# Kernel tuning notes

Hardware: AMD Instinct MI355X
Metric: run time of the kernel (lower is better)

The kernel has to match this reference:

```python
import jax, jax.numpy as jnp
import numpy as np

B, S, D_IN, D_H = 8, 2048, 768, 1024

def _linear_params(key, d_in, d_out):
    kw, kb = jax.random.split(key)
    bound = 1.0 / np.sqrt(d_in)
    W = jax.random.uniform(kw, (d_in, d_out), jnp.float32, -bound, bound)
    b = jax.random.uniform(kb, (d_out,), jnp.float32, -bound, bound)
    return W, b

def setup_inputs() -> dict:
    key = jax.random.key(0)
    ks = jax.random.split(key, 6)
    x = jax.random.normal(ks[0], (B, S, D_IN), jnp.float32)
    W1, b1 = _linear_params(ks[1], D_IN, D_H)
    Wq, bq = _linear_params(ks[2], D_H, D_H)
    Wk, bk = _linear_params(ks[3], D_H, D_H)
    Wv, bv = _linear_params(ks[4], D_H, D_H)
    W2, b2 = _linear_params(ks[5], D_H, D_H)
    Ws, bs = _linear_params(jax.random.fold_in(key, 7), D_IN, D_H)
    return {"x": x, "W1": W1, "b1": b1, "Wq": Wq, "bq": bq, "Wk": Wk, "bk": bk,
            "Wv": Wv, "bv": bv, "W2": W2, "b2": b2, "Ws": Ws, "bs": bs}

def reference(x, W1, b1, Wq, bq, Wk, bk, Wv, bv, W2, b2, Ws, bs):
    h = jax.nn.relu(x @ W1 + b1)                      # [B,S,D_H]
    q = h @ Wq + bq
    k = h @ Wk + bk
    v = h @ Wv + bv
    scale = 1.0 / jnp.sqrt(jnp.float32(h.shape[-1]))
    attn = jax.nn.softmax(jnp.einsum('bsd,btd->bst', q, k) * scale, axis=-1)
    h = jnp.einsum('bst,btd->bsd', attn, v)
    h = h + (x @ Ws + bs)                             # shortcut (input_dim != hidden_dim)
    return jax.nn.relu(h @ W2 + b2)
```

## Files before the change

### kernel.cpp

```cpp
#include <hip/hip_runtime.h>
#include <cstdint>
#include <cstddef>

#define BB   8
#define SS   2048
#define DIN  768
#define DHID 1024

typedef unsigned short u16;
typedef __bf16 bf16x8 __attribute__((ext_vector_type(8)));
typedef float  f32x4  __attribute__((ext_vector_type(4)));

__device__ __forceinline__ u16 f2bf(float f) {
  unsigned u = __float_as_uint(f);
  return (u16)((u + 0x7fffu + ((u >> 16) & 1u)) >> 16);
}
__device__ __forceinline__ float bf2f(u16 h) {
  return __uint_as_float((unsigned)h << 16);
}

#define GLOAD16(g, l)                                                         \
  __builtin_amdgcn_global_load_lds(                                           \
      (const __attribute__((address_space(1))) unsigned int*)(g),             \
      (__attribute__((address_space(3))) unsigned int*)(l), 16, 0, 0)

template <int OUT_MODE, bool RELU, bool HASRES>
__global__ __launch_bounds__(512, 2)
void gemm256(const u16* __restrict__ A, const u16* __restrict__ B,
             const float* __restrict__ bias, const u16* __restrict__ res,
             void* __restrict__ Cv, int M, int N, int K, float alpha,
             long strA, long strB, long strC) {
  __shared__ u16 sA[4][8192];
  __shared__ u16 sB[4][8192];

  const int nbx = gridDim.x, nby = gridDim.y;
  const long nwg  = (long)nbx * nby * gridDim.z;
  const long orig = blockIdx.x + (long)nbx * (blockIdx.y + (long)nby * blockIdx.z);
  const long per  = nwg >> 3;
  const long swz  = (orig & 7) * per + (orig >> 3);
  const int  bz   = (int)(swz / ((long)nbx * nby));
  const int  rem  = (int)(swz % ((long)nbx * nby));
  const int  by   = rem / nbx, bx = rem % nbx;

  A += (long)bz * strA;
  B += (long)bz * strB;

  const int tid  = threadIdx.x;
  const int lane = tid & 63;
  const int w    = tid >> 6;
  const int wr   = w >> 2;
  const int wc   = w & 3;
  const int bm0  = by * 256;
  const int bn0  = bx * 256;

  const int sr    = lane >> 2;
  const int clog  = ((lane & 3) * 8) ^ (((lane >> 2) & 6) << 2);
  const u16* AgBase = A + (long)(bm0 + w * 32 + sr) * K + clog;
  const u16* BgBase = B + (long)(bn0 + w * 32 + sr) * K + clog;

  const int fr = lane & 15;
  const int fk = (lane >> 4) * 8;
  const int ck = fk ^ ((fr & 6) << 2);

  f32x4 acc[8][4] = {};
  const int T = K >> 5;

  auto stage = [&](int t) {
    const int bf_ = t & 3;
    const long k0 = (long)t * 32;
    u16* la = &sA[bf_][(w * 32) * 32];
    u16* lb = &sB[bf_][(w * 32) * 32];
    GLOAD16(AgBase + k0,                 la);
    GLOAD16(AgBase + k0 + 16 * (long)K,  la + 16 * 32);
    GLOAD16(BgBase + k0,                 lb);
    GLOAD16(BgBase + k0 + 16 * (long)K,  lb + 16 * 32);
  };

  stage(0); stage(1); stage(2);
  asm volatile("s_waitcnt vmcnt(8)" ::: "memory");
  __builtin_amdgcn_s_barrier();
  __builtin_amdgcn_sched_barrier(0);

  for (int t = 0; t < T; ++t) {
    if (t + 3 < T) stage(t + 3);

    const int b = t & 3;
    bf16x8 af[8], bfv[4];
#pragma unroll
    for (int m = 0; m < 8; ++m)
      af[m] = *(const bf16x8*)(&sA[b][(wr * 128 + m * 16 + fr) * 32 + ck]);
#pragma unroll
    for (int n = 0; n < 4; ++n)
      bfv[n] = *(const bf16x8*)(&sB[b][(wc * 64 + n * 16 + fr) * 32 + ck]);

    asm volatile("s_waitcnt lgkmcnt(0)" ::: "memory");
    if (t + 3 < T)      asm volatile("s_waitcnt vmcnt(8)" ::: "memory");
    else if (t + 2 < T) asm volatile("s_waitcnt vmcnt(4)" ::: "memory");
    else                asm volatile("s_waitcnt vmcnt(0)" ::: "memory");
    __builtin_amdgcn_s_barrier();
    __builtin_amdgcn_sched_barrier(0);

    __builtin_amdgcn_s_setprio(1);
#pragma unroll
    for (int m = 0; m < 8; ++m)
#pragma unroll
      for (int n = 0; n < 4; ++n)
        acc[m][n] = __builtin_amdgcn_mfma_f32_16x16x32_bf16(af[m], bfv[n],
                                                            acc[m][n], 0, 0, 0);
    __builtin_amdgcn_s_setprio(0);
  }

#pragma unroll
  for (int m = 0; m < 8; ++m) {
    const int row0 = bm0 + wr * 128 + m * 16 + (lane >> 4) * 4;
#pragma unroll
    for (int n = 0; n < 4; ++n) {
      const int col = bn0 + wc * 64 + n * 16 + fr;
      f32x4 v = acc[m][n];
      const float bvv = bias ? bias[col] : 0.f;
#pragma unroll
      for (int r = 0; r < 4; ++r) {
        float val = v[r] * alpha + bvv;
        if (HASRES) val += bf2f(res[(long)(row0 + r) * N + col]);
        if (RELU)   val = fmaxf(val, 0.f);
        v[r] = val;
      }
      if (OUT_MODE == 0) {
        u16* C = (u16*)Cv + (long)bz * strC;
#pragma unroll
        for (int r = 0; r < 4; ++r)
          C[(long)(row0 + r) * N + col] = f2bf(v[r]);
      } else if (OUT_MODE == 1) {
        const int bb = row0 >> 11;
        const int s0 = row0 & 2047;
        u16* C = (u16*)Cv + (long)bb * (SS * DHID) + (long)col * SS + s0;
        ushort4 p;
        p.x = f2bf(v[0]); p.y = f2bf(v[1]); p.z = f2bf(v[2]); p.w = f2bf(v[3]);
        *(ushort4*)C = p;
      } else {
        float* C = (float*)Cv + (long)bz * strC;
#pragma unroll
        for (int r = 0; r < 4; ++r)
          C[(long)(row0 + r) * N + col] = v[r];
      }
    }
  }
}

__device__ __forceinline__ float waveReduce(float v, bool isMax) {
#pragma unroll
  for (int off = 32; off > 0; off >>= 1) {
    float o = __shfl_xor(v, off);
    v = isMax ? fmaxf(v, o) : (v + o);
  }
  return v;
}

__global__ __launch_bounds__(256)
void softmax2048b(u16* __restrict__ sc) {
  __shared__ float red[4];
  u16* row = sc + (size_t)blockIdx.x * 2048;
  const int tid = threadIdx.x;
  const int wv = tid >> 6, lane = tid & 63;

  uint4 raw = ((const uint4*)row)[tid];
  u16* us = (u16*)&raw;
  float f[8];
#pragma unroll
  for (int i = 0; i < 8; ++i) f[i] = bf2f(us[i]);

  float mx = f[0];
#pragma unroll
  for (int i = 1; i < 8; ++i) mx = fmaxf(mx, f[i]);
  mx = waveReduce(mx, true);
  if (lane == 0) red[wv] = mx;
  __syncthreads();
  mx = fmaxf(fmaxf(red[0], red[1]), fmaxf(red[2], red[3]));
  __syncthreads();

  float s = 0.f;
#pragma unroll
  for (int i = 0; i < 8; ++i) { f[i] = __expf(f[i] - mx); s += f[i]; }
  s = waveReduce(s, false);
  if (lane == 0) red[wv] = s;
  __syncthreads();
  s = red[0] + red[1] + red[2] + red[3];
  const float inv = 1.f / s;

#pragma unroll
  for (int i = 0; i < 8; ++i) us[i] = f2bf(f[i] * inv);
  ((uint4*)row)[tid] = raw;
}

__global__ __launch_bounds__(256)
void cvt8(const float* __restrict__ in, u16* __restrict__ out, long n) {
  long i = ((long)blockIdx.x * 256 + threadIdx.x) * 8;
  if (i >= n) return;
  float4 a = *(const float4*)(in + i);
  float4 b = *(const float4*)(in + i + 4);
  uint4 o;
  u16* us = (u16*)&o;
  us[0] = f2bf(a.x); us[1] = f2bf(a.y); us[2] = f2bf(a.z); us[3] = f2bf(a.w);
  us[4] = f2bf(b.x); us[5] = f2bf(b.y); us[6] = f2bf(b.z); us[7] = f2bf(b.w);
  *(uint4*)(out + i) = o;
}

__global__ __launch_bounds__(256)
void wtrans(const float* __restrict__ W, u16* __restrict__ WT, int K, int N) {
  __shared__ float t[32][33];
  const int tx = threadIdx.x & 31, ty = threadIdx.x >> 5;
  const int n0 = blockIdx.x * 32, k0 = blockIdx.y * 32;
#pragma unroll
  for (int r = 0; r < 32; r += 8)
    t[ty + r][tx] = W[(long)(k0 + ty + r) * N + n0 + tx];
  __syncthreads();
#pragma unroll
  for (int r = 0; r < 32; r += 8)
    WT[(long)(n0 + ty + r) * K + k0 + tx] = f2bf(t[tx][ty + r]);
}

extern "C" void kernel_launch(void* const* d_in, const int* in_sizes, int n_in,
                              void* d_out, int out_size, void* d_ws, size_t ws_size,
                              hipStream_t stream) {
  const float* x  = (const float*)d_in[0];
  const float* W1 = (const float*)d_in[1];
  const float* b1 = (const float*)d_in[2];
  const float* Wq = (const float*)d_in[3];
  const float* bq = (const float*)d_in[4];
  const float* Wk = (const float*)d_in[5];
  const float* bk = (const float*)d_in[6];
  const float* Wv = (const float*)d_in[7];
  const float* bv = (const float*)d_in[8];
  const float* W2 = (const float*)d_in[9];
  const float* b2 = (const float*)d_in[10];
  const float* Wsm = (const float*)d_in[11];
  const float* bs = (const float*)d_in[12];
  float* out = (float*)d_out;

  const long M   = (long)BB * SS;
  const long MD  = M * DHID;
  const long SD  = (long)SS * DHID;
  const long SSq = (long)SS * SS;
  const long NX  = M * DIN;

  u16* wsb = (u16*)d_ws;
  u16* xb  = wsb;
  u16* W1T = xb  + NX;
  u16* WqT = W1T + (long)DHID * DIN;
  u16* WkT = WqT + (long)DHID * DHID;
  u16* WvT = WkT + (long)DHID * DHID;
  u16* W2T = WvT + (long)DHID * DHID;
  u16* WsT = W2T + (long)DHID * DHID;
  u16* h   = WsT + (long)DHID * DIN;
  u16* q   = h + MD;
  u16* k   = q + MD;
  u16* scores = k + MD;
  u16* vT  = (u16*)d_out;

  long avail = (long)(ws_size / 2) - (scores - wsb);
  int nb = (int)(avail / SSq);
  if (nb > BB) nb = BB;
  if (nb < 1) nb = 1;

  cvt8<<<(unsigned)((NX / 8 + 255) / 256), 256, 0, stream>>>(x, xb, NX);
  wtrans<<<dim3(DHID / 32, DIN / 32), 256, 0, stream>>>(W1, W1T, DIN, DHID);
  wtrans<<<dim3(DHID / 32, DHID / 32), 256, 0, stream>>>(Wq, WqT, DHID, DHID);
  wtrans<<<dim3(DHID / 32, DHID / 32), 256, 0, stream>>>(Wk, WkT, DHID, DHID);
  wtrans<<<dim3(DHID / 32, DHID / 32), 256, 0, stream>>>(Wv, WvT, DHID, DHID);
  wtrans<<<dim3(DHID / 32, DHID / 32), 256, 0, stream>>>(W2, W2T, DHID, DHID);
  wtrans<<<dim3(DHID / 32, DIN / 32), 256, 0, stream>>>(Wsm, WsT, DIN, DHID);

  const dim3 gMain(DHID / 256, M / 256, 1);

  gemm256<0, true, false><<<gMain, 512, 0, stream>>>(
      xb, W1T, b1, nullptr, h, (int)M, DHID, DIN, 1.f, 0, 0, 0);
  gemm256<0, false, false><<<gMain, 512, 0, stream>>>(
      h, WqT, bq, nullptr, q, (int)M, DHID, DHID, 1.f, 0, 0, 0);
  gemm256<0, false, false><<<gMain, 512, 0, stream>>>(
      h, WkT, bk, nullptr, k, (int)M, DHID, DHID, 1.f, 0, 0, 0);
  gemm256<1, false, false><<<gMain, 512, 0, stream>>>(
      h, WvT, bv, nullptr, vT, (int)M, DHID, DHID, 1.f, 0, 0, 0);

  const float scale = 0.03125f;
  for (int b0 = 0; b0 < BB; b0 += nb) {
    const int cb = (b0 + nb <= BB) ? nb : (BB - b0);
    gemm256<0, false, false><<<dim3(SS / 256, SS / 256, cb), 512, 0, stream>>>(
        q + (long)b0 * SD, k + (long)b0 * SD, nullptr, nullptr, scores,
        SS, SS, DHID, scale, SD, SD, SSq);
    softmax2048b<<<cb * SS, 256, 0, stream>>>(scores);
    gemm256<0, false, false><<<dim3(DHID / 256, SS / 256, cb), 512, 0, stream>>>(
        scores, vT + (long)b0 * SD, nullptr, nullptr, h + (long)b0 * SD,
        SS, DHID, SS, 1.f, SSq, SD, SD);
  }

  gemm256<0, false, true><<<gMain, 512, 0, stream>>>(
      xb, WsT, bs, h, q, (int)M, DHID, DIN, 1.f, 0, 0, 0);

  gemm256<2, true, false><<<gMain, 512, 0, stream>>>(
      q, W2T, b2, nullptr, out, (int)M, DHID, DHID, 1.f, 0, 0, 0);
}
```

Measured before the change: 602.2 us.

## Restructure GEMM main loop into double-buffered 64-K stages with interleaved quarter-tile MFMA phases

Replaces the 4-deep 32-K circular LDS buffer with a 2-slot buffer of 64-K steps, each split into two 32-K halves. Each half is computed in two MFMA phases, and the next tile's A and B loads are issued between phases, so global-to-LDS traffic is spread across the iteration. Fragment registers are halved (af[4] instead of af[8]) and the launch-bounds occupancy hint of 2 is dropped. This should cut register pressure and overlap loads with compute more finely. The cost is many more barriers per iteration and a shallower prefetch distance, which may expose memory latency.

```diff
diff --git a/kernel.cpp b/kernel.cpp
--- a/kernel.cpp
+++ b/kernel.cpp
@@ -24,14 +24,17 @@
       (const __attribute__((address_space(1))) unsigned int*)(g),             \
       (__attribute__((address_space(3))) unsigned int*)(l), 16, 0, 0)
 
+#define SB0()  __builtin_amdgcn_sched_barrier(0)
+#define BAR()  __builtin_amdgcn_s_barrier()
+
 template <int OUT_MODE, bool RELU, bool HASRES>
-__global__ __launch_bounds__(512, 2)
+__global__ __launch_bounds__(512)
 void gemm256(const u16* __restrict__ A, const u16* __restrict__ B,
              const float* __restrict__ bias, const u16* __restrict__ res,
              void* __restrict__ Cv, int M, int N, int K, float alpha,
              long strA, long strB, long strC) {
-  __shared__ u16 sA[4][8192];
-  __shared__ u16 sB[4][8192];
+  __shared__ u16 sA[2][2][8192];
+  __shared__ u16 sB[2][2][8192];
 
   const int nbx = gridDim.x, nby = gridDim.y;
   const long nwg  = (long)nbx * nby * gridDim.z;
@@ -53,61 +56,111 @@
   const int bm0  = by * 256;
   const int bn0  = bx * 256;
 
-  const int sr    = lane >> 2;
-  const int clog  = ((lane & 3) * 8) ^ (((lane >> 2) & 6) << 2);
-  const u16* AgBase = A + (long)(bm0 + w * 32 + sr) * K + clog;
-  const u16* BgBase = B + (long)(bn0 + w * 32 + sr) * K + clog;
+  const int sr   = lane >> 2;
+  const int clog = ((lane & 3) * 8) ^ (((lane >> 2) & 6) << 2);
+  const u16* Ag = A + (long)(bm0 + w * 32 + sr) * K + clog;
+  const u16* Bg = B + (long)(bn0 + w * 32 + sr) * K + clog;
 
   const int fr = lane & 15;
   const int fk = (lane >> 4) * 8;
   const int ck = fk ^ ((fr & 6) << 2);
+  const int aoff = (wr * 128 + fr) * 32 + ck;
+  const int boff = (wc * 64  + fr) * 32 + ck;
+
+  auto stageA = [&](int slot, int ks, int t) {
+    u16* d = &sA[slot][ks][(w * 32) * 32];
+    const u16* g = Ag + (long)t * 64 + ks * 32;
+    GLOAD16(g, d);
+    GLOAD16(g + 16 * (long)K, d + 512);
+  };
+  auto stageB = [&](int slot, int ks, int t) {
+    u16* d = &sB[slot][ks][(w * 32) * 32];
+    const u16* g = Bg + (long)t * 64 + ks * 32;
+    GLOAD16(g, d);
+    GLOAD16(g + 16 * (long)K, d + 512);
+  };
 
   f32x4 acc[8][4] = {};
-  const int T = K >> 5;
-
-  auto stage = [&](int t) {
-    const int bf_ = t & 3;
-    const long k0 = (long)t * 32;
-    u16* la = &sA[bf_][(w * 32) * 32];
-    u16* lb = &sB[bf_][(w * 32) * 32];
-    GLOAD16(AgBase + k0,                 la);
-    GLOAD16(AgBase + k0 + 16 * (long)K,  la + 16 * 32);
-    GLOAD16(BgBase + k0,                 lb);
-    GLOAD16(BgBase + k0 + 16 * (long)K,  lb + 16 * 32);
-  };
-
-  stage(0); stage(1); stage(2);
-  asm volatile("s_waitcnt vmcnt(8)" ::: "memory");
-  __builtin_amdgcn_s_barrier();
-  __builtin_amdgcn_sched_barrier(0);
+  bf16x8 af[4], bfv[4];
+  const int T = K >> 6;
+
+  stageA(0, 0, 0); stageB(0, 0, 0); stageA(0, 1, 0); stageB(0, 1, 0);
+  asm volatile("s_waitcnt vmcnt(4)" ::: "memory");
+  BAR(); SB0();
 
   for (int t = 0; t < T; ++t) {
-    if (t + 3 < T) stage(t + 3);
-
-    const int b = t & 3;
-    bf16x8 af[8], bfv[4];
-#pragma unroll
-    for (int m = 0; m < 8; ++m)
-      af[m] = *(const bf16x8*)(&sA[b][(wr * 128 + m * 16 + fr) * 32 + ck]);
+    const int s = t & 1, s1 = s ^ 1;
+    const bool pf = (t + 1 < T);
+
+#pragma unroll
+    for (int m = 0; m < 4; ++m)
+      af[m] = *(const bf16x8*)(&sA[s][0][aoff + m * 512]);
 #pragma unroll
     for (int n = 0; n < 4; ++n)
-      bfv[n] = *(const bf16x8*)(&sB[b][(wc * 64 + n * 16 + fr) * 32 + ck]);
-
-    asm volatile("s_waitcnt lgkmcnt(0)" ::: "memory");
-    if (t + 3 < T)      asm volatile("s_waitcnt vmcnt(8)" ::: "memory");
-    else if (t + 2 < T) asm volatile("s_waitcnt vmcnt(4)" ::: "memory");
-    else                asm volatile("s_waitcnt vmcnt(0)" ::: "memory");
-    __builtin_amdgcn_s_barrier();
-    __builtin_amdgcn_sched_barrier(0);
-
+      bfv[n] = *(const bf16x8*)(&sB[s][0][boff + n * 512]);
+    if (pf) stageA(s1, 0, t + 1);
+    SB0(); BAR(); SB0();
     __builtin_amdgcn_s_setprio(1);
 #pragma unroll
-    for (int m = 0; m < 8; ++m)
+    for (int m = 0; m < 4; ++m)
 #pragma unroll
       for (int n = 0; n < 4; ++n)
         acc[m][n] = __builtin_amdgcn_mfma_f32_16x16x32_bf16(af[m], bfv[n],
                                                             acc[m][n], 0, 0, 0);
     __builtin_amdgcn_s_setprio(0);
+    BAR(); SB0();
+
+#pragma unroll
+    for (int m = 0; m < 4; ++m)
+      af[m] = *(const bf16x8*)(&sA[s][0][aoff + (m + 4) * 512]);
+    if (pf) stageB(s1, 0, t + 1);
+    SB0(); BAR(); SB0();
+    __builtin_amdgcn_s_setprio(1);
+#pragma unroll
+    for (int m = 0; m < 4; ++m)
+#pragma unroll
+      for (int n = 0; n < 4; ++n)
+        acc[m + 4][n] = __builtin_amdgcn_mfma_f32_16x16x32_bf16(af[m], bfv[n],
+                                                                acc[m + 4][n], 0, 0, 0);
+    __builtin_amdgcn_s_setprio(0);
+    if (pf) asm volatile("s_waitcnt vmcnt(4)" ::: "memory");
+    else    asm volatile("s_waitcnt vmcnt(0)" ::: "memory");
+    BAR(); SB0();
+
+#pragma unroll
+    for (int m = 0; m < 4; ++m)
+      af[m] = *(const bf16x8*)(&sA[s][1][aoff + m * 512]);
+#pragma unroll
+    for (int n = 0; n < 4; ++n)
+      bfv[n] = *(const bf16x8*)(&sB[s][1][boff + n * 512]);
+    if (pf) stageA(s1, 1, t + 1);
+    SB0(); BAR(); SB0();
+    __builtin_amdgcn_s_setprio(1);
+#pragma unroll
+    for (int m = 0; m < 4; ++m)
+#pragma unroll
+      for (int n = 0; n < 4; ++n)
+        acc[m][n] = __builtin_amdgcn_mfma_f32_16x16x32_bf16(af[m], bfv[n],
+                                                            acc[m][n], 0, 0, 0);
+    __builtin_amdgcn_s_setprio(0);
+    BAR(); SB0();
+
+#pragma unroll
+    for (int m = 0; m < 4; ++m)
+      af[m] = *(const bf16x8*)(&sA[s][1][aoff + (m + 4) * 512]);
+    if (pf) stageB(s1, 1, t + 1);
+    SB0(); BAR(); SB0();
+    __builtin_amdgcn_s_setprio(1);
+#pragma unroll
+    for (int m = 0; m < 4; ++m)
+#pragma unroll
+      for (int n = 0; n < 4; ++n)
+        acc[m + 4][n] = __builtin_amdgcn_mfma_f32_16x16x32_bf16(af[m], bfv[n],
+                                                                acc[m + 4][n], 0, 0, 0);
+    __builtin_amdgcn_s_setprio(0);
+    if (pf) asm volatile("s_waitcnt vmcnt(4)" ::: "memory");
+    else    asm volatile("s_waitcnt vmcnt(0)" ::: "memory");
+    BAR(); SB0();
   }
 
 #pragma unroll
```

Result: faster. 549.6 us (-8.7%).
